# Kernel optimization log

Measured on AMD Instinct MI355X. Metric: run time of the kernel, lower is better.

Reference implementation:

```python
import jax, jax.numpy as jnp
import numpy as np

K = 16  # neighbors (module's self.k)


def _gather(points, idx):
    # points (B,C,N), idx (B,M[,k]) -> (B,C,M[,k])
    return jax.vmap(lambda p, i: p[:, i])(points, idx)


def _fps(xyz, nsample):
    # furthest point sampling on xyz (B,3,N) -> idx (B,nsample) int32
    B, _, N = xyz.shape

    def body(carry, _):
        dists, last = carry
        lp = jnp.take_along_axis(xyz, last[:, None, None], axis=2)  # (B,3,1)
        d = jnp.sum((xyz - lp) ** 2, axis=1)  # (B,N)
        dists = jnp.minimum(dists, d)
        nxt = jnp.argmax(dists, axis=1).astype(jnp.int32)
        return (dists, nxt), nxt

    init_idx = jnp.zeros((B,), dtype=jnp.int32)
    init_d = jnp.full((B, N), jnp.finfo(xyz.dtype).max, xyz.dtype)
    _, rest = jax.lax.scan(body, (init_d, init_idx), None, length=nsample - 1)
    return jnp.concatenate([init_idx[None], rest], axis=0).T  # (B,nsample)


def _knn(query, points, k):
    # query (B,C,M), points (B,C,N): k nearest in feature space
    d = (jnp.sum(query ** 2, axis=1)[:, :, None]
         + jnp.sum(points ** 2, axis=1)[:, None, :]
         - 2.0 * jnp.einsum('bcm,bcn->bmn', query, points))  # (B,M,N)
    _, idx = jax.lax.top_k(-d, k)  # (B,M,k)
    return _gather(points, idx), idx  # (B,C,M,k), (B,M,k)


def _conv1x1(W, b, y):
    # y (B,Cin,M,k), W (Cout,Cin) -> (B,Cout,M,k)
    return jnp.einsum('oi,bimk->bomk', W, y) + b[None, :, None, None]


def setup_inputs() -> dict:
    key = jax.random.key(0)
    ks = jax.random.split(key, 8)
    B, C, N = 4, 64, 8192
    g = 64
    return {
        'x': jax.random.normal(ks[0], (B, C, N), jnp.float32),
        'xyz': jax.random.normal(ks[1], (B, 3, N), jnp.float32),
        'W0': jax.random.normal(ks[2], (g, 2 * C), jnp.float32) * 0.05,
        'b0': jax.random.normal(ks[3], (g,), jnp.float32) * 0.05,
        'W1': jax.random.normal(ks[4], (g, C + g), jnp.float32) * 0.05,
        'b1': jax.random.normal(ks[5], (g,), jnp.float32) * 0.05,
        'W2': jax.random.normal(ks[6], (g, C + 2 * g), jnp.float32) * 0.05,
        'b2': jax.random.normal(ks[7], (g,), jnp.float32) * 0.05,
        'nsample': 2048,
    }


def reference(x, xyz, W0, b0, W1, b1, W2, b2, nsample):
    # furthest point sample on coordinates, gather sampled features
    sampled_idx = _fps(xyz, nsample)              # (B,M)
    sampled_xyz = _gather(xyz, sampled_idx)       # (B,3,M)
    sampled_x = _gather(x, sampled_idx)           # (B,C,M)
    # local graph: k+1 NN in feature space, drop self
    knn_pt, _ = _knn(sampled_x, x, K + 1)
    knn_pt = knn_pt[..., 1:]                      # (B,C,M,K)
    center = sampled_x[..., None]                 # (B,C,M,1)
    center_k = jnp.broadcast_to(center, knn_pt.shape)
    edge = jnp.concatenate([center_k, knn_pt - center_k], axis=1)  # (B,2C,M,K)
    # dense edge conv cascade
    y = jnp.concatenate([jax.nn.relu(_conv1x1(W0, b0, edge)), center_k], axis=1)
    y = jnp.concatenate([jax.nn.relu(_conv1x1(W1, b1, y)), y], axis=1)
    y = jnp.concatenate([_conv1x1(W2, b2, y), y], axis=1)
    y = jnp.max(y, axis=-1)                       # (B, C+3*g, M)
    return (y, sampled_xyz, sampled_idx)
```

## Files before the change

kernel.cpp:

```cpp
#include <hip/hip_runtime.h>
#include <hip/hip_bf16.h>
#include <stdint.h>

typedef unsigned long long u64;
typedef unsigned int u32;
typedef unsigned short u16;

#define B_   4
#define C_   64
#define N_   8192
#define M_   2048
#define KNB  16
#define FLT_MAX_ 3.402823466e+38f
#define SMEM_SZ 87312
#define NSPLIT 8

__device__ __forceinline__ int clampN(int v) {
    return v < 0 ? 0 : (v > N_ - 1 ? N_ - 1 : v);
}


__device__ __forceinline__ void pin4(float4& v) {
    asm volatile("" : "+v"(v.x), "+v"(v.y), "+v"(v.z), "+v"(v.w));
}

__device__ __forceinline__ float wave_fmax_dpp(float v) {
    float t;
    t = __int_as_float(__builtin_amdgcn_update_dpp(0, __float_as_int(v), 0x111, 0xf, 0xf, true)); v = fmaxf(v, t);
    t = __int_as_float(__builtin_amdgcn_update_dpp(0, __float_as_int(v), 0x112, 0xf, 0xf, true)); v = fmaxf(v, t);
    t = __int_as_float(__builtin_amdgcn_update_dpp(0, __float_as_int(v), 0x114, 0xf, 0xf, true)); v = fmaxf(v, t);
    t = __int_as_float(__builtin_amdgcn_update_dpp(0, __float_as_int(v), 0x118, 0xf, 0xf, true)); v = fmaxf(v, t);
    t = __int_as_float(__builtin_amdgcn_update_dpp(0, __float_as_int(v), 0x142, 0xa, 0xf, true)); v = fmaxf(v, t);
    t = __int_as_float(__builtin_amdgcn_update_dpp(0, __float_as_int(v), 0x143, 0xc, 0xf, true)); v = fmaxf(v, t);
    return __int_as_float(__builtin_amdgcn_readlane(__float_as_int(v), 63));
}

#define FPS_STEP(PX, PY, PZ, DD, J)                                          \
    {                                                                        \
        float dx = __fsub_rn((PX), lx);                                      \
        float dy = __fsub_rn((PY), ly);                                      \
        float dz = __fsub_rn((PZ), lz);                                      \
        float d = __fadd_rn(__fadd_rn(__fmul_rn(dx, dx), __fmul_rn(dy, dy)), \
                            __fmul_rn(dz, dz));                              \
        float nd = fminf((DD), d);                                           \
        (DD) = nd;                                                           \
        bool gt = nd > fm;                                                   \
        fm = gt ? nd : fm;                                                   \
        fj = gt ? (J) : fj;                                                  \
        fx = gt ? (PX) : fx;                                                 \
        fy = gt ? (PY) : fy;                                                 \
        fz = gt ? (PZ) : fz;                                                 \
    }

__global__ void init_kernel(u32* __restrict__ scratch) {
    if (threadIdx.x < 272) scratch[threadIdx.x] = 0;
}

__global__ __launch_bounds__(512, 2) void mega_kernel(
    const float* __restrict__ xyz, const float* __restrict__ x,
    const float* __restrict__ W0, const float* __restrict__ W1,
    const float* __restrict__ W2, u16* __restrict__ idx_ws,
    float* __restrict__ pnorm_ws, float* __restrict__ wt,
    float* __restrict__ out1, float* __restrict__ out2,
    u16* __restrict__ nbr_ws,
    u32* __restrict__ part_hi, u16* __restrict__ part_lo,
    u32* __restrict__ flags, u32* __restrict__ done) {
    const int bid = blockIdx.x;
    const int tid = threadIdx.x;
    __shared__ __align__(16) char SM[SMEM_SZ];

    if (bid < 4) {
        const int b = bid;
        const int lane = tid & 63;
        const int w = tid >> 6;
        const float* xb = xyz + b * 3 * N_;
        const int n0 = tid * 16;

        float4* red4 = (float4*)SM;
        int*    redi = (int*)(SM + 256);
        u16*    hist = (u16*)(SM + 320);

        float4 px[4], py[4], pz[4], dd[4];
#pragma unroll
        for (int j4 = 0; j4 < 4; ++j4) {
            px[j4] = *(const float4*)(xb + n0 + j4 * 4);
            py[j4] = *(const float4*)(xb + N_ + n0 + j4 * 4);
            pz[j4] = *(const float4*)(xb + 2 * N_ + n0 + j4 * 4);
            pin4(px[j4]); pin4(py[j4]); pin4(pz[j4]);
            dd[j4] = make_float4(FLT_MAX_, FLT_MAX_, FLT_MAX_, FLT_MAX_);
        }

        int cur = 0;
        float lx = xb[0], ly = xb[N_], lz = xb[2 * N_];
        if (tid == 0) { idx_ws[b * M_ + 0] = 0; hist[0] = 0; }

        for (int s = 1; s < M_; ++s) {
            float fm = -1.0f, fx = 0.f, fy = 0.f, fz = 0.f;
            int fj = 0;
#pragma unroll
            for (int j4 = 0; j4 < 4; ++j4) {
                FPS_STEP(px[j4].x, py[j4].x, pz[j4].x, dd[j4].x, j4 * 4 + 0);
                FPS_STEP(px[j4].y, py[j4].y, pz[j4].y, dd[j4].y, j4 * 4 + 1);
                FPS_STEP(px[j4].z, py[j4].z, pz[j4].z, dd[j4].z, j4 * 4 + 2);
                FPS_STEP(px[j4].w, py[j4].w, pz[j4].w, dd[j4].w, j4 * 4 + 3);
            }
            float wm = wave_fmax_dpp(fm);
            u64 bal = __ballot(fm == wm);
            int winlane = (int)__ffsll(bal) - 1;
            const int par = s & 1;
            if (lane == winlane) {
                red4[(par << 3) + w] = make_float4(wm, fx, fy, fz);
                redi[(par << 3) + w] = n0 + fj;
            }
            __syncthreads();
            float4 p0 = red4[par << 3];
            float g = p0.x; float nlx = p0.y, nly = p0.z, nlz = p0.w;
            int ncur = redi[par << 3];
#pragma unroll
            for (int ww = 1; ww < 8; ++ww) {
                float4 p = red4[(par << 3) + ww];
                int id = redi[(par << 3) + ww];
                bool gt = p.x > g;
                g = gt ? p.x : g;
                nlx = gt ? p.y : nlx; nly = gt ? p.z : nly; nlz = gt ? p.w : nlz;
                ncur = gt ? id : ncur;
            }
            lx = nlx; ly = nly; lz = nlz; cur = ncur;
            if (tid == 0) {
                idx_ws[b * M_ + s] = (u16)cur; hist[s] = (u16)cur;
                if ((s & 63) == 63)
                    __hip_atomic_store(&flags[b], (u32)s, __ATOMIC_RELEASE,
                                       __HIP_MEMORY_SCOPE_AGENT);
            }
        }

        __syncthreads();
        for (int m = tid; m < M_; m += 512) {
            int idx = (int)hist[m];
            out2[b * M_ + m] = (float)idx;
            out1[(b * 3 + 0) * M_ + m] = xb[idx];
            out1[(b * 3 + 1) * M_ + m] = xb[N_ + idx];
            out1[(b * 3 + 2) * M_ + m] = xb[2 * N_ + idx];
        }
        return;
    }

    if (bid < 68) {
        int gid = (bid - 4) * 512 + tid;
        int bb = gid >> 13, n = gid & 8191;
        const float* xb = x + bb * C_ * N_ + n;
        float acc = 0.f;
#pragma unroll 16
        for (int c = 0; c < C_; ++c) { float v = xb[c * N_]; acc = fmaf(v, v, acc); }
        pnorm_ws[gid] = acc;
        __syncthreads();
        if (tid == 0)
            __hip_atomic_fetch_add(&flags[4], 1u, __ATOMIC_RELEASE,
                                   __HIP_MEMORY_SCOPE_AGENT);
        return;
    }

    if (bid < 124) {
        int e = (bid - 68) * 512 + tid;
        if (e < 8192) {
            int i = e >> 6, o = e & 63;
            wt[e] = W0[o * 128 + i];
        } else if (e < 16384) {
            int e2 = e - 8192; int i = e2 >> 6, o = e2 & 63;
            wt[8192 + e2] = W1[o * 128 + i];
        } else {
            int e2 = e - 16384; int i = e2 >> 6, o = e2 & 63;
            wt[16384 + e2] = W2[o * 192 + i];
        }
        return;
    }

    {
        const int kid = bid - 124;
        const int grp = kid >> 5;
        const int b   = (kid >> 3) & 3;
        const int sp  = kid & 7;
        const int m0  = grp * 32;

        float* pt    = (float*)SM;
        float* spn   = (float*)(SM + 17408);
        u64*   lists = (u64*)(SM + 17664);
        int*   lastp = (int*)(SM + 87296);

        if (tid == 0) {
            while (__hip_atomic_load(&flags[4], __ATOMIC_ACQUIRE,
                                     __HIP_MEMORY_SCOPE_AGENT) < 64u)
                __builtin_amdgcn_s_sleep(2);
            const u32 need = (u32)(m0 + 31);
            while (__hip_atomic_load(&flags[b], __ATOMIC_ACQUIRE,
                                     __HIP_MEMORY_SCOPE_AGENT) < need)
                __builtin_amdgcn_s_sleep(2);
        }
        __syncthreads();

        const int q = tid & 31, sub = tid >> 5;
        const int m = m0 + q;
        const float* xb = x + b * C_ * N_;
        const int self = clampN((int)idx_ws[b * M_ + m]);

        float4 qv[16];
#pragma unroll
        for (int c4 = 0; c4 < 16; ++c4) {
            qv[c4].x = xb[(c4 * 4 + 0) * N_ + self];
            qv[c4].y = xb[(c4 * 4 + 1) * N_ + self];
            qv[c4].z = xb[(c4 * 4 + 2) * N_ + self];
            qv[c4].w = xb[(c4 * 4 + 3) * N_ + self];
        }
        const float qn = pnorm_ws[b * N_ + self];

        u64* L = lists + tid * 17;
#pragma unroll
        for (int j = 0; j < 17; ++j) L[j] = ~0ULL;
        u64 worst = ~0ULL;

        const int tF = sp * 16, tL = tF + 16;
        const int cA = tid >> 4, nqA = tid & 15, csA = cA ^ (nqA << 2);
        const int eB = tid + 512;
        const int cB = eB >> 4, nqB = eB & 15, csB = cB ^ (nqB << 2);
        const float* pA = xb + cA * N_ + nqA * 4;
        const float* pB = xb + cB * N_ + nqB * 4;

        float4 s0 = *(const float4*)(pA + tF * 64);
        float4 s1 = *(const float4*)(pB + tF * 64);
        float sv = (tid < 64) ? pnorm_ws[b * N_ + tF * 64 + tid] : 0.f;

        for (int t = tF; t < tL; ++t) {
            __syncthreads();
            pt[(nqA * 4 + 0) * 68 + csA] = s0.x;
            pt[(nqA * 4 + 1) * 68 + csA] = s0.y;
            pt[(nqA * 4 + 2) * 68 + csA] = s0.z;
            pt[(nqA * 4 + 3) * 68 + csA] = s0.w;
            pt[(nqB * 4 + 0) * 68 + csB] = s1.x;
            pt[(nqB * 4 + 1) * 68 + csB] = s1.y;
            pt[(nqB * 4 + 2) * 68 + csB] = s1.z;
            pt[(nqB * 4 + 3) * 68 + csB] = s1.w;
            if (tid < 64) spn[tid] = sv;
            float4 n0 = make_float4(0.f, 0.f, 0.f, 0.f), n1 = n0;
            float nv = 0.f;
            if (t + 1 < tL) {
                n0 = *(const float4*)(pA + (t + 1) * 64);
                n1 = *(const float4*)(pB + (t + 1) * 64);
                if (tid < 64) nv = pnorm_ws[b * N_ + (t + 1) * 64 + tid];
            }
            __syncthreads();
            const int nb0 = t * 64;
#pragma unroll
            for (int pp = 0; pp < 4; ++pp) {
                int nl = sub * 4 + pp;
                const float* pvbase = pt + nl * 68;
                const int rsw = (nl >> 2) << 2;
                float a0 = 0.f, a1 = 0.f, a2 = 0.f, a3 = 0.f;
#pragma unroll
                for (int c4 = 0; c4 < 16; ++c4) {
                    float4 p = *(const float4*)(pvbase + (((c4 << 2) ^ rsw)));
                    a0 = fmaf(qv[c4].x, p.x, a0);
                    a1 = fmaf(qv[c4].y, p.y, a1);
                    a2 = fmaf(qv[c4].z, p.z, a2);
                    a3 = fmaf(qv[c4].w, p.w, a3);
                }
                float dot = (a0 + a1) + (a2 + a3);
                float d = qn + spn[nl] - 2.0f * dot;
                u32 db = __float_as_uint(d);
                db = (db & 0x80000000u) ? ~db : (db | 0x80000000u);
                u64 key = ((u64)db << 32) | (u32)(nb0 + nl);
                if (key < worst) {
                    int j = 16;
                    while (j > 0 && L[j - 1] > key) { L[j] = L[j - 1]; --j; }
                    L[j] = key;
                    worst = L[16];
                }
            }
            s0 = n0; s1 = n1; sv = nv;
        }
        __syncthreads();
        if (tid < 32) {
            int pos[16];
#pragma unroll
            for (int s2 = 0; s2 < 16; ++s2) pos[s2] = 0;
            const u32 base = (u32)(((b * M_ + m0 + tid) * NSPLIT + sp) * 17);
            for (int r = 0; r < 17; ++r) {
                u64 best = ~0ULL; int bs = 0;
#pragma unroll
                for (int s2 = 0; s2 < 16; ++s2) {
                    u64 k2 = (pos[s2] < 17) ? lists[(tid + 32 * s2) * 17 + pos[s2]] : ~0ULL;
                    if (k2 < best) { best = k2; bs = s2; }
                }
#pragma unroll
                for (int s2 = 0; s2 < 16; ++s2) pos[s2] += (s2 == bs) ? 1 : 0;
                part_hi[base + r] = (u32)(best >> 32);
                part_lo[base + r] = (u16)(best & 0xFFFFu);
            }
        }
        __syncthreads();
        if (tid == 0) {
            u32 old = __hip_atomic_fetch_add(&done[b * 64 + grp], 1u,
                                             __ATOMIC_ACQ_REL,
                                             __HIP_MEMORY_SCOPE_AGENT);
            *lastp = (old == (u32)(NSPLIT - 1)) ? 1 : 0;
        }
        __syncthreads();

        if (*lastp && tid < 32) {
            const int gid = b * M_ + m0 + tid;
            const u32* ph = part_hi + (u64)gid * NSPLIT * 17;
            const u16* pl = part_lo + (u64)gid * NSPLIT * 17;
            int pos[NSPLIT];
#pragma unroll
            for (int s = 0; s < NSPLIT; ++s) pos[s] = 0;
            u16* outp = nbr_ws + gid * KNB;
            for (int r = 0; r < 17; ++r) {
                u64 best = ~0ULL; int bs = 0;
#pragma unroll
                for (int s = 0; s < NSPLIT; ++s) {
                    int p = pos[s];
                    u64 k = (p < 17) ? ((((u64)ph[s * 17 + p]) << 32) | (u64)pl[s * 17 + p])
                                     : ~0ULL;
                    if (k < best) { best = k; bs = s; }
                }
#pragma unroll
                for (int s = 0; s < NSPLIT; ++s) pos[s] += (s == bs) ? 1 : 0;
                if (r > 0) outp[r - 1] = (u16)clampN((int)(best & 0xFFFFu));
            }
        }
    }
}

__device__ __forceinline__ void mm_tile(float a[4][4], const float* __restrict__ w,
                                        const float* __restrict__ s, int ni) {
#pragma unroll 8
    for (int i = 0; i < ni; ++i) {
        const float4 w4 = *(const float4*)(w + i * 64);
        const float4 e4 = *(const float4*)(s + i * 64);
        a[0][0] = fmaf(w4.x, e4.x, a[0][0]);
        a[0][1] = fmaf(w4.x, e4.y, a[0][1]);
        a[0][2] = fmaf(w4.x, e4.z, a[0][2]);
        a[0][3] = fmaf(w4.x, e4.w, a[0][3]);
        a[1][0] = fmaf(w4.y, e4.x, a[1][0]);
        a[1][1] = fmaf(w4.y, e4.y, a[1][1]);
        a[1][2] = fmaf(w4.y, e4.z, a[1][2]);
        a[1][3] = fmaf(w4.y, e4.w, a[1][3]);
        a[2][0] = fmaf(w4.z, e4.x, a[2][0]);
        a[2][1] = fmaf(w4.z, e4.y, a[2][1]);
        a[2][2] = fmaf(w4.z, e4.z, a[2][2]);
        a[2][3] = fmaf(w4.z, e4.w, a[2][3]);
        a[3][0] = fmaf(w4.w, e4.x, a[3][0]);
        a[3][1] = fmaf(w4.w, e4.y, a[3][1]);
        a[3][2] = fmaf(w4.w, e4.z, a[3][2]);
        a[3][3] = fmaf(w4.w, e4.w, a[3][3]);
    }
}

__global__ __launch_bounds__(256) void conv_kernel(const float* __restrict__ x,
                                                   const u16* __restrict__ idx_ws,
                                                   const u16* __restrict__ nbr_ws,
                                                   const float* __restrict__ wt,
                                                   const float* __restrict__ bias0,
                                                   const float* __restrict__ bias1,
                                                   const float* __restrict__ bias2,
                                                   float* __restrict__ out0) {
    __shared__ float E[128 * 64];
    __shared__ float H0[64 * 64];

    const int tid = threadIdx.x;
    const int b = blockIdx.x >> 9;
    const int m0 = (blockIdx.x & 511) * 4;
    const float* xb = x + b * C_ * N_;

    {
        const int col = tid & 63;
        const int half = tid >> 6;
        const int m = m0 + (col >> 4);
        const int k = col & 15;
        const int selfm = clampN((int)idx_ws[b * M_ + m]);
        const int nbr = clampN((int)nbr_ws[(b * M_ + m) * KNB + k]);
#pragma unroll
        for (int c2 = 0; c2 < 16; ++c2) {
            int c = half * 16 + c2;
            float ctr = xb[c * N_ + selfm];
            float nb = xb[c * N_ + nbr];
            E[c * 64 + col] = ctr;
            E[(64 + c) * 64 + col] = __fsub_rn(nb, ctr);
        }
    }
    __syncthreads();

    const int o0 = (tid >> 4) * 4;
    const int c0 = (tid & 15) * 4;
    float a[4][4];

    {
        float4 bb = *(const float4*)(bias0 + o0);
        a[0][0] = a[0][1] = a[0][2] = a[0][3] = bb.x;
        a[1][0] = a[1][1] = a[1][2] = a[1][3] = bb.y;
        a[2][0] = a[2][1] = a[2][2] = a[2][3] = bb.z;
        a[3][0] = a[3][1] = a[3][2] = a[3][3] = bb.w;
        mm_tile(a, wt + o0, E + c0, 128);
#pragma unroll
        for (int oo = 0; oo < 4; ++oo) {
            float4 v = make_float4(fmaxf(a[oo][0], 0.f), fmaxf(a[oo][1], 0.f),
                                   fmaxf(a[oo][2], 0.f), fmaxf(a[oo][3], 0.f));
            *(float4*)(H0 + (o0 + oo) * 64 + c0) = v;
        }
    }
    __syncthreads();

    {
        float4 bb = *(const float4*)(bias1 + o0);
        a[0][0] = a[0][1] = a[0][2] = a[0][3] = bb.x;
        a[1][0] = a[1][1] = a[1][2] = a[1][3] = bb.y;
        a[2][0] = a[2][1] = a[2][2] = a[2][3] = bb.z;
        a[3][0] = a[3][1] = a[3][2] = a[3][3] = bb.w;
        mm_tile(a, wt + 8192 + o0, H0 + c0, 64);
        mm_tile(a, wt + 8192 + 64 * 64 + o0, E + c0, 64);
#pragma unroll
        for (int oo = 0; oo < 4; ++oo) {
            float4 v = make_float4(fmaxf(a[oo][0], 0.f), fmaxf(a[oo][1], 0.f),
                                   fmaxf(a[oo][2], 0.f), fmaxf(a[oo][3], 0.f));
            *(float4*)(E + (64 + o0 + oo) * 64 + c0) = v;
        }
    }
    __syncthreads();

    {
        float4 bb = *(const float4*)(bias2 + o0);
        a[0][0] = a[0][1] = a[0][2] = a[0][3] = bb.x;
        a[1][0] = a[1][1] = a[1][2] = a[1][3] = bb.y;
        a[2][0] = a[2][1] = a[2][2] = a[2][3] = bb.z;
        a[3][0] = a[3][1] = a[3][2] = a[3][3] = bb.w;
        mm_tile(a, wt + 16384 + o0, E + 64 * 64 + c0, 64);
        mm_tile(a, wt + 16384 + 64 * 64 + o0, H0 + c0, 64);
        mm_tile(a, wt + 16384 + 128 * 64 + o0, E + c0, 64);
    }

#pragma unroll
    for (int r = 1; r < 4; ++r) {
        int e = tid + r * 256;
        int ch = e >> 2, mloc = e & 3;
        int colb = mloc * 16;
        float v;
        if (ch < 128) {
            const float* row = E + (64 + (ch - 64)) * 64 + colb;
            v = row[0];
#pragma unroll
            for (int k = 1; k < 16; ++k) v = fmaxf(v, row[k]);
        } else if (ch < 192) {
            const float* row = H0 + (ch - 128) * 64 + colb;
            v = row[0];
#pragma unroll
            for (int k = 1; k < 16; ++k) v = fmaxf(v, row[k]);
        } else {
            v = E[(ch - 192) * 64 + colb];
        }
        out0[((b * 256 + ch) << 11) + m0 + mloc] = v;
    }
    __syncthreads();

    {
#pragma unroll
        for (int oo = 0; oo < 4; ++oo) {
            float4 v = make_float4(a[oo][0], a[oo][1], a[oo][2], a[oo][3]);
            *(float4*)(E + (64 + o0 + oo) * 64 + c0) = v;
        }
    }
    __syncthreads();

    {
        int ch = tid >> 2, mloc = tid & 3;
        int colb = mloc * 16;
        const float* row = E + (64 + ch) * 64 + colb;
        float v = row[0];
#pragma unroll
        for (int k = 1; k < 16; ++k) v = fmaxf(v, row[k]);
        out0[((b * 256 + ch) << 11) + m0 + mloc] = v;
    }
}

extern "C" void kernel_launch(void* const* d_in, const int* in_sizes, int n_in,
                              void* d_out, int out_size, void* d_ws, size_t ws_size,
                              hipStream_t stream) {
    const float* x   = (const float*)d_in[0];
    const float* xyz = (const float*)d_in[1];
    const float* W0  = (const float*)d_in[2];
    const float* b0  = (const float*)d_in[3];
    const float* W1  = (const float*)d_in[4];
    const float* b1  = (const float*)d_in[5];
    const float* W2  = (const float*)d_in[6];
    const float* b2  = (const float*)d_in[7];

    float* out  = (float*)d_out;
    float* out0 = out;
    float* out1 = out + 4 * 256 * 2048;
    float* out2 = out1 + 4 * 3 * 2048;
    u32*   scratch = (u32*)out0;
    u32*   flags   = scratch;
    u32*   done    = scratch + 16;
    u32*   part_hi = scratch + 272;
    u16*   part_lo = (u16*)(part_hi + 8192 * NSPLIT * 17);

    char* ws = (char*)d_ws;
    u16*   idx_ws   = (u16*)ws;
    u16*   nbr_ws   = (u16*)(ws + 16384);
    float* pnorm_ws = (float*)(ws + 278528);
    float* wt_ws    = (float*)(ws + 409600);

    init_kernel<<<1, 512, 0, stream>>>(scratch);
    mega_kernel<<<2172, 512, 0, stream>>>(xyz, x, W0, W1, W2,
                                          idx_ws, pnorm_ws, wt_ws,
                                          out1, out2, nbr_ws,
                                          part_hi, part_lo, flags, done);
    conv_kernel<<<2048, 256, 0, stream>>>(x, idx_ws, nbr_ws, wt_ws,
                                          b0, b1, b2, out0);
}
```

Baseline: 2.391 ms.

## Split late KNN groups across more blocks to shorten the FPS-dependent tail

KNN query groups whose sample indices are produced last by the sequential FPS (groups 60-63) are now split 32 ways over the point set instead of 8. Each of those blocks scans 4 tiles instead of 16. The aim is to shrink the critical-path tail that waits on the final FPS samples. The cost is more blocks, a separate partial-result buffer, and a 32-way merge in the last block for those groups.

Measured after the change: 2.442 ms. 1.02x slower.

```diff
diff --git a/kernel.cpp b/kernel.cpp
--- a/kernel.cpp
+++ b/kernel.cpp
@@ -13,7 +13,7 @@
 #define KNB  16
 #define FLT_MAX_ 3.402823466e+38f
 #define SMEM_SZ 87312
-#define NSPLIT 8
+#define GLATE 60
 
 __device__ __forceinline__ int clampN(int v) {
     return v < 0 ? 0 : (v > N_ - 1 ? N_ - 1 : v);
@@ -63,7 +63,8 @@
     float* __restrict__ pnorm_ws, float* __restrict__ wt,
     float* __restrict__ out1, float* __restrict__ out2,
     u16* __restrict__ nbr_ws,
-    u32* __restrict__ part_hi, u16* __restrict__ part_lo,
+    u32* __restrict__ part_hi_e, u16* __restrict__ part_lo_e,
+    u32* __restrict__ part_hi_l, u16* __restrict__ part_lo_l,
     u32* __restrict__ flags, u32* __restrict__ done) {
     const int bid = blockIdx.x;
     const int tid = threadIdx.x;
@@ -177,10 +178,20 @@
 
     {
         const int kid = bid - 124;
-        const int grp = kid >> 5;
-        const int b   = (kid >> 3) & 3;
-        const int sp  = kid & 7;
-        const int m0  = grp * 32;
+        int grp, b, sp, nspl, tps;
+        if (kid < 1920) {
+            grp = kid >> 5;
+            b   = (kid >> 3) & 3;
+            sp  = kid & 7;
+            nspl = 8; tps = 16;
+        } else {
+            int k2 = kid - 1920;
+            grp = GLATE + (k2 >> 7);
+            b   = (k2 >> 5) & 3;
+            sp  = k2 & 31;
+            nspl = 32; tps = 4;
+        }
+        const int m0 = grp * 32;
 
         float* pt    = (float*)SM;
         float* spn   = (float*)(SM + 17408);
@@ -218,7 +229,7 @@
         for (int j = 0; j < 17; ++j) L[j] = ~0ULL;
         u64 worst = ~0ULL;
 
-        const int tF = sp * 16, tL = tF + 16;
+        const int tF = sp * tps, tL = tF + tps;
         const int cA = tid >> 4, nqA = tid & 15, csA = cA ^ (nqA << 2);
         const int eB = tid + 512;
         const int cB = eB >> 4, nqB = eB & 15, csB = cB ^ (nqB << 2);
@@ -282,7 +293,16 @@
             int pos[16];
 #pragma unroll
             for (int s2 = 0; s2 < 16; ++s2) pos[s2] = 0;
-            const u32 base = (u32)(((b * M_ + m0 + tid) * NSPLIT + sp) * 17);
+            u32 base;
+            if (nspl == 8) {
+                const u32 slot = (u32)(b * 1920 + m0 + tid);
+                base = (slot * 8 + (u32)sp) * 17;
+            } else {
+                const u32 lslot = (u32)(b * 128 + (m0 - 1920) + tid);
+                base = (lslot * 32 + (u32)sp) * 17;
+            }
+            u32* ph = (nspl == 8) ? part_hi_e : part_hi_l;
+            u16* pl = (nspl == 8) ? part_lo_e : part_lo_l;
             for (int r = 0; r < 17; ++r) {
                 u64 best = ~0ULL; int bs = 0;
 #pragma unroll
@@ -292,8 +312,8 @@
                 }
 #pragma unroll
                 for (int s2 = 0; s2 < 16; ++s2) pos[s2] += (s2 == bs) ? 1 : 0;
-                part_hi[base + r] = (u32)(best >> 32);
-                part_lo[base + r] = (u16)(best & 0xFFFFu);
+                ph[base + r] = (u32)(best >> 32);
+                pl[base + r] = (u16)(best & 0xFFFFu);
             }
         }
         __syncthreads();
@@ -301,30 +321,52 @@
             u32 old = __hip_atomic_fetch_add(&done[b * 64 + grp], 1u,
                                              __ATOMIC_ACQ_REL,
                                              __HIP_MEMORY_SCOPE_AGENT);
-            *lastp = (old == (u32)(NSPLIT - 1)) ? 1 : 0;
+            *lastp = (old == (u32)(nspl - 1)) ? 1 : 0;
         }
         __syncthreads();
 
         if (*lastp && tid < 32) {
-            const int gid = b * M_ + m0 + tid;
-            const u32* ph = part_hi + (u64)gid * NSPLIT * 17;
-            const u16* pl = part_lo + (u64)gid * NSPLIT * 17;
-            int pos[NSPLIT];
-#pragma unroll
-            for (int s = 0; s < NSPLIT; ++s) pos[s] = 0;
-            u16* outp = nbr_ws + gid * KNB;
-            for (int r = 0; r < 17; ++r) {
-                u64 best = ~0ULL; int bs = 0;
-#pragma unroll
-                for (int s = 0; s < NSPLIT; ++s) {
-                    int p = pos[s];
-                    u64 k = (p < 17) ? ((((u64)ph[s * 17 + p]) << 32) | (u64)pl[s * 17 + p])
-                                     : ~0ULL;
-                    if (k < best) { best = k; bs = s; }
+            u16* outp = nbr_ws + (b * M_ + m0 + tid) * KNB;
+            if (nspl == 8) {
+                const u32 slot = (u32)(b * 1920 + m0 + tid);
+                const u32* ph = part_hi_e + (u64)slot * 8 * 17;
+                const u16* pl = part_lo_e + (u64)slot * 8 * 17;
+                int pos[8];
+#pragma unroll
+                for (int s = 0; s < 8; ++s) pos[s] = 0;
+                for (int r = 0; r < 17; ++r) {
+                    u64 best = ~0ULL; int bs = 0;
+#pragma unroll
+                    for (int s = 0; s < 8; ++s) {
+                        int p = pos[s];
+                        u64 k = (p < 17) ? ((((u64)ph[s * 17 + p]) << 32) | (u64)pl[s * 17 + p])
+                                         : ~0ULL;
+                        if (k < best) { best = k; bs = s; }
+                    }
+#pragma unroll
+                    for (int s = 0; s < 8; ++s) pos[s] += (s == bs) ? 1 : 0;
+                    if (r > 0) outp[r - 1] = (u16)clampN((int)(best & 0xFFFFu));
                 }
-#pragma unroll
-                for (int s = 0; s < NSPLIT; ++s) pos[s] += (s == bs) ? 1 : 0;
-                if (r > 0) outp[r - 1] = (u16)clampN((int)(best & 0xFFFFu));
+            } else {
+                const u32 lslot = (u32)(b * 128 + (m0 - 1920) + tid);
+                const u32* ph = part_hi_l + (u64)lslot * 32 * 17;
+                const u16* pl = part_lo_l + (u64)lslot * 32 * 17;
+                int pos[32];
+#pragma unroll
+                for (int s = 0; s < 32; ++s) pos[s] = 0;
+                for (int r = 0; r < 17; ++r) {
+                    u64 best = ~0ULL; int bs = 0;
+#pragma unroll
+                    for (int s = 0; s < 32; ++s) {
+                        int p = pos[s];
+                        u64 k = (p < 17) ? ((((u64)ph[s * 17 + p]) << 32) | (u64)pl[s * 17 + p])
+                                         : ~0ULL;
+                        if (k < best) { best = k; bs = s; }
+                    }
+#pragma unroll
+                    for (int s = 0; s < 32; ++s) pos[s] += (s == bs) ? 1 : 0;
+                    if (r > 0) outp[r - 1] = (u16)clampN((int)(best & 0xFFFFu));
+                }
             }
         }
     }
@@ -496,11 +538,13 @@
     float* out0 = out;
     float* out1 = out + 4 * 256 * 2048;
     float* out2 = out1 + 4 * 3 * 2048;
-    u32*   scratch = (u32*)out0;
-    u32*   flags   = scratch;
-    u32*   done    = scratch + 16;
-    u32*   part_hi = scratch + 272;
-    u16*   part_lo = (u16*)(part_hi + 8192 * NSPLIT * 17);
+    u32*   scratch   = (u32*)out0;
+    u32*   flags     = scratch;
+    u32*   done      = scratch + 16;
+    u32*   part_hi_e = scratch + 272;
+    u16*   part_lo_e = (u16*)(part_hi_e + 7680 * 136);
+    u32*   part_hi_l = (u32*)((char*)part_lo_e + 7680 * 136 * 2);
+    u16*   part_lo_l = (u16*)(part_hi_l + 512 * 544);
 
     char* ws = (char*)d_ws;
     u16*   idx_ws   = (u16*)ws;
@@ -509,10 +553,12 @@
     float* wt_ws    = (float*)(ws + 409600);
 
     init_kernel<<<1, 512, 0, stream>>>(scratch);
-    mega_kernel<<<2172, 512, 0, stream>>>(xyz, x, W0, W1, W2,
+    mega_kernel<<<2556, 512, 0, stream>>>(xyz, x, W0, W1, W2,
                                           idx_ws, pnorm_ws, wt_ws,
                                           out1, out2, nbr_ws,
-                                          part_hi, part_lo, flags, done);
+                                          part_hi_e, part_lo_e,
+                                          part_hi_l, part_lo_l,
+                                          flags, done);
     conv_kernel<<<2048, 256, 0, stream>>>(x, idx_ws, nbr_ws, wt_ws,
                                           b0, b1, b2, out0);
 }
```
